# Optimization experiments

Measured on AMD Instinct MI355X. Metric: run time of the kernel, lower is better.

## Reference

```python
import jax, jax.numpy as jnp
import numpy as np

B, N, F_DIM, E, C = 8, 16384, 64, 262144, 10
BN_EPS = 1e-5


def setup_inputs() -> dict:
    key = jax.random.key(0)
    ks = jax.random.split(key, 10)
    s = 1.0 / np.sqrt(F_DIM)
    return {
        "x": jax.random.normal(ks[0], (B, N, F_DIM), jnp.float32),
        "edge_src": jax.random.randint(ks[1], (B, E), 0, N, jnp.int32),
        "edge_dst": jax.random.randint(ks[2], (B, E), 0, N, jnp.int32),
        "W1": jax.random.normal(ks[3], (F_DIM, F_DIM), jnp.float32) * s,
        "b1": jax.random.normal(ks[4], (F_DIM,), jnp.float32) * 0.01,
        "W2": jax.random.normal(ks[5], (F_DIM, F_DIM), jnp.float32) * s,
        "b2": jax.random.normal(ks[6], (F_DIM,), jnp.float32) * 0.01,
        "bn_gamma": jnp.ones((F_DIM,), jnp.float32),
        "bn_beta": jnp.zeros((F_DIM,), jnp.float32),
        "lin_W": jax.random.normal(ks[7], (C, N * F_DIM), jnp.float32) * (1.0 / np.sqrt(N * F_DIM)),
        "lin_b": jax.random.normal(ks[8], (C,), jnp.float32) * 0.01,
    }


def _graph_conv(x, src, dst, W, b):
    # DGL GraphConv, norm='both', in_feats == out_feats (aggregate-first path):
    # h = D_in^{-1/2} * A * (D_out^{-1/2} * x) @ W + b, degrees clamped to >= 1.
    ones = jnp.ones((src.shape[0],), x.dtype)
    deg_out = jnp.maximum(jax.ops.segment_sum(ones, src, num_segments=N), 1.0)
    deg_in = jnp.maximum(jax.ops.segment_sum(ones, dst, num_segments=N), 1.0)
    xs = x * jax.lax.rsqrt(deg_out)[:, None]          # [N, F]
    agg = jax.ops.segment_sum(xs[src], dst, num_segments=N)  # gather + scatter-add
    rst = agg * jax.lax.rsqrt(deg_in)[:, None]
    return rst @ W + b


def reference(x, edge_src, edge_dst, W1, b1, W2, b2, bn_gamma, bn_beta, lin_W, lin_b):
    conv = jax.vmap(_graph_conv, in_axes=(0, 0, 0, None, None))
    h = jax.nn.relu(conv(x, edge_src, edge_dst, W1, b1))  # conv1 + relu
    # dropout p=0.0 (eval): identity
    h = conv(h, edge_src, edge_dst, W2, b2)               # conv2 -> [B, N, F]
    # BatchNorm1d over channel F (torch normalizes over B and N in training mode)
    mean = jnp.mean(h, axis=(0, 1))
    var = jnp.var(h, axis=(0, 1))
    h = bn_gamma * (h - mean) * jax.lax.rsqrt(var + BN_EPS) + bn_beta
    flat = h.reshape(B, N * F_DIM)
    return flat @ lin_W.T + lin_b                         # [B, C]
```

## Files before the change

### kernel.cpp

```cpp
#include <hip/hip_runtime.h>

#define B_     8
#define N_     16384
#define F_     64
#define E_     262144
#define C_     10
#define NF_    (N_ * F_)
#define BN_    (B_ * N_)
#define BNF_   (B_ * N_ * F_)
#define BE_    (B_ * E_)
#define CAP_   48
#define CHUNK_ 4096
#define NCH_   (E_ / CHUNK_)
#define NW_    (N_ / 4)
#define NSB_   2048
#define NFB_   1024
#define EPS_   1e-5f

typedef _Float16 h8 __attribute__((ext_vector_type(8)));
typedef _Float16 h4 __attribute__((ext_vector_type(4)));

__global__ __launch_bounds__(256) void k_count(const int* __restrict__ src,
                                               const int* __restrict__ dst,
                                               unsigned int* __restrict__ partO,
                                               unsigned int* __restrict__ partI) {
    __shared__ unsigned int pO[NW_];
    __shared__ unsigned int pI[NW_];
    int t = threadIdx.x;
    int b = blockIdx.x & 7, c = blockIdx.x >> 3;
    for (int i = t; i < NW_; i += 256) { pO[i] = 0; pI[i] = 0; }
    __syncthreads();
    const int* sb = src + (size_t)b * E_ + (size_t)c * CHUNK_;
    const int* db = dst + (size_t)b * E_ + (size_t)c * CHUNK_;
    for (int i = t; i < CHUNK_; i += 256) {
        int s = sb[i], d = db[i];
        atomicAdd(&pO[s >> 2], 1u << ((s & 3) * 8));
        atomicAdd(&pI[d >> 2], 1u << ((d & 3) * 8));
    }
    __syncthreads();
    size_t base = (size_t)(b * NCH_ + c) * NW_;
    for (int i = t; i < NW_; i += 256) {
        partO[base + i] = pO[i];
        partI[base + i] = pI[i];
    }
}

__global__ __launch_bounds__(256) void k_offsets(const unsigned int* __restrict__ partO,
                                                 const unsigned int* __restrict__ partI,
                                                 unsigned int* __restrict__ baseArr,
                                                 float* __restrict__ degOr,
                                                 float* __restrict__ degIr,
                                                 int* __restrict__ cntI_g) {
    int gw = blockIdx.x * 256 + threadIdx.x;
    int b = gw >> 12;
    int rw = gw & 4095;
    unsigned int sumI = 0, sumO = 0;
    for (int c = 0; c < NCH_; ++c) {
        size_t idx = (size_t)(b * NCH_ + c) * NW_ + rw;
        unsigned int wI = partI[idx];
        baseArr[idx] = sumI;
        sumI += wI;
        sumO += partO[idx];
    }
    int row0 = gw * 4;
#pragma unroll
    for (int r = 0; r < 4; ++r) {
        unsigned int ci = (sumI >> (r * 8)) & 0xFFu;
        unsigned int co = (sumO >> (r * 8)) & 0xFFu;
        degIr[row0 + r] = rsqrtf(fmaxf((float)ci, 1.0f));
        degOr[row0 + r] = rsqrtf(fmaxf((float)co, 1.0f));
        cntI_g[row0 + r] = (int)ci;
    }
}

__global__ __launch_bounds__(256) void k_fill(const int* __restrict__ src,
                                              const int* __restrict__ dst,
                                              const unsigned int* __restrict__ baseArr,
                                              unsigned short* __restrict__ csr) {
    __shared__ unsigned int cur[NW_];
    __shared__ unsigned int bw[NW_];
    int t = threadIdx.x;
    int b = blockIdx.x & 7, c = blockIdx.x >> 3;
    size_t pbase = (size_t)(b * NCH_ + c) * NW_;
    for (int i = t; i < NW_; i += 256) { cur[i] = 0; bw[i] = baseArr[pbase + i]; }
    __syncthreads();
    const int* sb = src + (size_t)b * E_ + (size_t)c * CHUNK_;
    const int* db = dst + (size_t)b * E_ + (size_t)c * CHUNK_;
    unsigned short* cb = csr + (size_t)b * N_ * CAP_;
    for (int i = t; i < CHUNK_; i += 256) {
        int s = sb[i], d = db[i];
        unsigned int sh = (d & 3) * 8;
        unsigned int old = atomicAdd(&cur[d >> 2], 1u << sh);
        unsigned int pos = ((old >> sh) & 0xFFu) + ((bw[d >> 2] >> sh) & 0xFFu);
        if (pos < CAP_) cb[d * CAP_ + pos] = (unsigned short)s;
    }
}

template <bool SCALE, bool IN16, bool OUT16>
__global__ __launch_bounds__(256) void k_mmd(const float* __restrict__ in32,
                                             const _Float16* __restrict__ in16,
                                             const float* __restrict__ W,
                                             const float* __restrict__ rs,
                                             float* __restrict__ out32,
                                             _Float16* __restrict__ out16) {
    __shared__ float Wl[4096];
    __shared__ float4 rows[16][16];
    int t = threadIdx.x;
    int b = blockIdx.x & 7;
    int rowg = b * N_ + (blockIdx.x >> 3) * 16;
    for (int i = t; i < 1024; i += 256) ((float4*)Wl)[i] = ((const float4*)W)[i];
    {
        int rr = t >> 4, g = t & 15;
        if (IN16) {
            h4 hv = *(const h4*)(in16 + (size_t)(rowg + rr) * 64 + g * 4);
            rows[rr][g] = make_float4((float)hv[0], (float)hv[1], (float)hv[2], (float)hv[3]);
        } else {
            rows[rr][g] = ((const float4*)(in32 + (size_t)(rowg + rr) * 64))[g];
        }
    }
    __syncthreads();
    int f = t & 63;
    int wv = t >> 6;
    float a0 = 0.0f, a1 = 0.0f, a2 = 0.0f, a3 = 0.0f;
#pragma unroll
    for (int kg = 0; kg < 16; ++kg) {
        float4 r0 = rows[wv * 4 + 0][kg];
        float4 r1 = rows[wv * 4 + 1][kg];
        float4 r2 = rows[wv * 4 + 2][kg];
        float4 r3 = rows[wv * 4 + 3][kg];
        float w0 = Wl[(kg * 4 + 0) * 64 + f];
        float w1 = Wl[(kg * 4 + 1) * 64 + f];
        float w2 = Wl[(kg * 4 + 2) * 64 + f];
        float w3 = Wl[(kg * 4 + 3) * 64 + f];
        a0 = fmaf(r0.x, w0, a0); a0 = fmaf(r0.y, w1, a0); a0 = fmaf(r0.z, w2, a0); a0 = fmaf(r0.w, w3, a0);
        a1 = fmaf(r1.x, w0, a1); a1 = fmaf(r1.y, w1, a1); a1 = fmaf(r1.z, w2, a1); a1 = fmaf(r1.w, w3, a1);
        a2 = fmaf(r2.x, w0, a2); a2 = fmaf(r2.y, w1, a2); a2 = fmaf(r2.z, w2, a2); a2 = fmaf(r2.w, w3, a2);
        a3 = fmaf(r3.x, w0, a3); a3 = fmaf(r3.y, w1, a3); a3 = fmaf(r3.z, w2, a3); a3 = fmaf(r3.w, w3, a3);
    }
    int r0i = rowg + wv * 4;
    if (SCALE) {
        a0 *= rs[r0i]; a1 *= rs[r0i + 1]; a2 *= rs[r0i + 2]; a3 *= rs[r0i + 3];
    }
    if (OUT16) {
        out16[(size_t)(r0i + 0) * 64 + f] = (_Float16)a0;
        out16[(size_t)(r0i + 1) * 64 + f] = (_Float16)a1;
        out16[(size_t)(r0i + 2) * 64 + f] = (_Float16)a2;
        out16[(size_t)(r0i + 3) * 64 + f] = (_Float16)a3;
    } else {
        out32[(size_t)(r0i + 0) * 64 + f] = a0;
        out32[(size_t)(r0i + 1) * 64 + f] = a1;
        out32[(size_t)(r0i + 2) * 64 + f] = a2;
        out32[(size_t)(r0i + 3) * 64 + f] = a3;
    }
}

template <bool CONV1>
__global__ __launch_bounds__(256, 6) void k_gat(
        const int* __restrict__ cnt, const unsigned short* __restrict__ csr,
        const _Float16* __restrict__ z, const float* __restrict__ degIr,
        const float* __restrict__ degOr, const float* __restrict__ bias,
        _Float16* __restrict__ out16, float* __restrict__ out32) {
    int t = threadIdx.x;
    int lane = t & 63;
    int wave = t >> 6;
    int c8 = lane & 7;
    int b = blockIdx.x & 7;
    int row = (blockIdx.x >> 3) * 32 + wave * 8 + (lane >> 3);
    int wid = b * N_ + row;
    const _Float16* zb = z + (size_t)b * NF_;
    int lb = lane & 56;
    int ho = c8 * 8;

    int n = cnt[wid];
    if (n > CAP_) n = CAP_;
    size_t cb = (size_t)wid * CAP_;
    int e0 = csr[cb + c8] & 0x3FFF;
    int e1 = csr[cb + 8 + c8] & 0x3FFF;
    int e2 = csr[cb + 16 + c8] & 0x3FFF;
    int e3 = csr[cb + 24 + c8] & 0x3FFF;
    int e4 = csr[cb + 32 + c8] & 0x3FFF;
    int e5 = csr[cb + 40 + c8] & 0x3FFF;
    float dIr = degIr[wid];
    float4 bv0 = *(const float4*)(bias + ho);
    float4 bv1 = *(const float4*)(bias + ho + 4);
    int m = n;
    m = max(m, __shfl_xor(m, 8));
    m = max(m, __shfl_xor(m, 16));
    m = max(m, __shfl_xor(m, 32));

    float af[8];
#pragma unroll
    for (int i = 0; i < 8; ++i) af[i] = 0.0f;

#define SEG(EREG, KOFF)                                                        \
    {                                                                          \
        int rem = n - (KOFF);                                                  \
        h8 v[8];                                                               \
        _Pragma("unroll")                                                      \
        for (int jj = 0; jj < 8; ++jj) {                                       \
            int s = __shfl(EREG, lb + jj);                                     \
            h8 vv = {};                                                        \
            if (jj < rem) vv = *(const h8*)(zb + s * 64 + ho);                 \
            v[jj] = vv;                                                        \
        }                                                                      \
        h8 s0 = v[0] + v[1], s1 = v[2] + v[3];                                 \
        h8 s2 = v[4] + v[5], s3 = v[6] + v[7];                                 \
        h8 s4 = s0 + s1, s5 = s2 + s3;                                         \
        h8 s6 = s4 + s5;                                                       \
        _Pragma("unroll")                                                      \
        for (int i = 0; i < 8; ++i) af[i] += (float)s6[i];                     \
    }

    SEG(e0, 0)
    if (m > 8)  SEG(e1, 8)
    if (m > 16) SEG(e2, 16)
    if (m > 24) SEG(e3, 24)
    if (m > 32) SEG(e4, 32)
    if (m > 40) SEG(e5, 40)
#undef SEG

    float bb[8] = {bv0.x, bv0.y, bv0.z, bv0.w, bv1.x, bv1.y, bv1.z, bv1.w};
    if (CONV1) {
        float po = degOr[wid];
        h8 ov;
#pragma unroll
        for (int i = 0; i < 8; ++i) {
            ov[i] = (_Float16)(fmaxf(fmaf(af[i], dIr, bb[i]), 0.0f) * po);
        }
        *(h8*)(out16 + (size_t)wid * 64 + ho) = ov;
    } else {
        float4 o0, o1;
        o0.x = fmaf(af[0], dIr, bb[0]); o0.y = fmaf(af[1], dIr, bb[1]);
        o0.z = fmaf(af[2], dIr, bb[2]); o0.w = fmaf(af[3], dIr, bb[3]);
        o1.x = fmaf(af[4], dIr, bb[4]); o1.y = fmaf(af[5], dIr, bb[5]);
        o1.z = fmaf(af[6], dIr, bb[6]); o1.w = fmaf(af[7], dIr, bb[7]);
        float* op = out32 + (size_t)wid * 64 + ho;
        *(float4*)op = o0;
        *(float4*)(op + 4) = o1;
    }
}

__global__ __launch_bounds__(256) void k_stats2(const float* __restrict__ h,
                                                float* __restrict__ part) {
    int t = threadIdx.x;
    int base = blockIdx.x * (BNF_ / NSB_);
    float s = 0.0f, q = 0.0f;
#pragma unroll 4
    for (int k = 0; k < 16; ++k) {
        float v = h[(size_t)base + k * 256 + t];
        s += v;
        q += v * v;
    }
    __shared__ float ls[256], lq[256];
    ls[t] = s;
    lq[t] = q;
    __syncthreads();
    if (t < 64) {
        s = ls[t] + ls[t + 64] + ls[t + 128] + ls[t + 192];
        q = lq[t] + lq[t + 64] + lq[t + 128] + lq[t + 192];
        float* p = part + (size_t)blockIdx.x * 128;
        p[t] = s;
        p[64 + t] = q;
    }
}

__global__ __launch_bounds__(256) void k_red(const float* __restrict__ part,
                                             float* __restrict__ stats2) {
    __shared__ float sred[256];
    int t = threadIdx.x;
    int half = t >> 7;
    int s = t & 127;
    int r0 = blockIdx.x * (NSB_ / 32);
    float acc = 0.0f;
    for (int k = 0; k < NSB_ / 32 / 2; ++k) {
        acc += part[(size_t)(r0 + k * 2 + half) * 128 + s];
    }
    sred[t] = acc;
    __syncthreads();
    if (t < 128) stats2[blockIdx.x * 128 + t] = sred[t] + sred[t + 128];
}

__global__ void k_bnfin(const float* __restrict__ stats2, const float* __restrict__ gamma,
                        const float* __restrict__ beta, float* __restrict__ sc,
                        float* __restrict__ sh) {
    int f = threadIdx.x;
    if (f < 64) {
        float sum = 0.0f, sq = 0.0f;
        for (int j = 0; j < 32; ++j) {
            sum += stats2[j * 128 + f];
            sq  += stats2[j * 128 + 64 + f];
        }
        float inv = 1.0f / (float)BN_;
        float mean = sum * inv;
        float var  = sq * inv - mean * mean;
        float s = gamma[f] * rsqrtf(var + EPS_);
        sc[f] = s;
        sh[f] = beta[f] - mean * s;
    }
}

__global__ __launch_bounds__(256) void k_final(
        const float* __restrict__ h, const float* __restrict__ linW,
        const float* __restrict__ sc, const float* __restrict__ sh,
        float* __restrict__ pf) {
    int t = threadIdx.x;
    int lane = t & 63;
    int wv = t >> 6;
    int b0 = wv * 2, b1 = wv * 2 + 1;
    int base = blockIdx.x * (NF_ / NFB_);
    float s = sc[lane], shv = sh[lane];
    float acc[C_][2];
#pragma unroll
    for (int c = 0; c < C_; ++c) { acc[c][0] = 0.0f; acc[c][1] = 0.0f; }

#pragma unroll 4
    for (int k = 0; k < 16; ++k) {
        int i = base + k * 64 + lane;
        float h0 = fmaf(h[(size_t)b0 * NF_ + i], s, shv);
        float h1 = fmaf(h[(size_t)b1 * NF_ + i], s, shv);
#pragma unroll
        for (int c = 0; c < C_; ++c) {
            float w = linW[(size_t)c * NF_ + i];
            acc[c][0] = fmaf(h0, w, acc[c][0]);
            acc[c][1] = fmaf(h1, w, acc[c][1]);
        }
    }

#pragma unroll
    for (int c = 0; c < C_; ++c) {
#pragma unroll
        for (int j = 0; j < 2; ++j) {
            float v = acc[c][j];
            v += __shfl_down(v, 32);
            v += __shfl_down(v, 16);
            v += __shfl_down(v, 8);
            v += __shfl_down(v, 4);
            v += __shfl_down(v, 2);
            v += __shfl_down(v, 1);
            acc[c][j] = v;
        }
    }
    if (lane == 0) {
        float* p = pf + (size_t)blockIdx.x * 80;
#pragma unroll
        for (int c = 0; c < C_; ++c) {
            p[b0 * C_ + c] = acc[c][0];
            p[b1 * C_ + c] = acc[c][1];
        }
    }
}

__global__ __launch_bounds__(64) void k_fsum(const float* __restrict__ pf,
                                             const float* __restrict__ linb,
                                             float* __restrict__ out) {
    int o = blockIdx.x;
    int lane = threadIdx.x;
    float acc = 0.0f;
#pragma unroll
    for (int k = 0; k < 16; ++k) {
        acc += pf[(size_t)(k * 64 + lane) * 80 + o];
    }
    acc += __shfl_down(acc, 32);
    acc += __shfl_down(acc, 16);
    acc += __shfl_down(acc, 8);
    acc += __shfl_down(acc, 4);
    acc += __shfl_down(acc, 2);
    acc += __shfl_down(acc, 1);
    if (lane == 0) out[o] = acc + linb[o % C_];
}

extern "C" void kernel_launch(void* const* d_in, const int* in_sizes, int n_in,
                              void* d_out, int out_size, void* d_ws, size_t ws_size,
                              hipStream_t stream) {
    const float* x        = (const float*)d_in[0];
    const int*   edge_src = (const int*)d_in[1];
    const int*   edge_dst = (const int*)d_in[2];
    const float* W1       = (const float*)d_in[3];
    const float* b1       = (const float*)d_in[4];
    const float* W2       = (const float*)d_in[5];
    const float* b2       = (const float*)d_in[6];
    const float* gamma    = (const float*)d_in[7];
    const float* beta     = (const float*)d_in[8];
    const float* linW     = (const float*)d_in[9];
    const float* linb     = (const float*)d_in[10];
    float* out = (float*)d_out;

    char* w = (char*)d_ws;
    float* degOr = (float*)w;           w += BN_ * 4;
    float* degIr = (float*)w;           w += BN_ * 4;
    int*   cntI  = (int*)w;             w += BN_ * 4;
    unsigned short* csr = (unsigned short*)w; w += (size_t)BN_ * CAP_ * 2;
    _Float16* z    = (_Float16*)w;      w += (size_t)BNF_ * 2;
    _Float16* h1z  = (_Float16*)w;      w += (size_t)BNF_ * 2;
    float* h2    = (float*)w;           w += (size_t)BNF_ * 4;
    float* statPart = (float*)w;        w += (size_t)NSB_ * 128 * 4;
    float* stats2 = (float*)w;          w += 32 * 128 * 4;
    float* pf    = (float*)w;           w += (size_t)NFB_ * 80 * 4;
    float* sc    = (float*)w;           w += 64 * 4;
    float* sh    = (float*)w;           w += 64 * 4;

    unsigned int* partO   = (unsigned int*)h2;
    unsigned int* partI   = partO + (size_t)B_ * NCH_ * NW_;
    unsigned int* baseArr = (unsigned int*)z;

    k_count<<<B_ * NCH_, 256, 0, stream>>>(edge_src, edge_dst, partO, partI);
    k_offsets<<<BN_ / 4 / 256, 256, 0, stream>>>(partO, partI, baseArr, degOr, degIr, cntI);
    k_fill<<<B_ * NCH_, 256, 0, stream>>>(edge_src, edge_dst, baseArr, csr);

    k_mmd<true, false, true><<<BN_ / 16, 256, 0, stream>>>(x, nullptr, W1, degOr, nullptr, z);
    k_gat<true><<<BN_ / 32, 256, 0, stream>>>(cntI, csr, z, degIr, degOr, b1, h1z, nullptr);

    k_mmd<false, true, true><<<BN_ / 16, 256, 0, stream>>>(nullptr, h1z, W2, nullptr, nullptr, z);
    k_gat<false><<<BN_ / 32, 256, 0, stream>>>(cntI, csr, z, degIr, nullptr, b2, nullptr, h2);

    k_stats2<<<NSB_, 256, 0, stream>>>(h2, statPart);
    k_red<<<32, 256, 0, stream>>>(statPart, stats2);
    k_bnfin<<<1, 64, 0, stream>>>(stats2, gamma, beta, sc, sh);
    k_final<<<NFB_, 256, 0, stream>>>(h2, linW, sc, sh, pf);
    k_fsum<<<80, 64, 0, stream>>>(pf, linb, out);
}
```

Before: 280.8 us.

## Use MFMA f16 for feature transforms and fuse BN stats into conv2 gather

```diff
diff --git a/kernel.cpp b/kernel.cpp
--- a/kernel.cpp
+++ b/kernel.cpp
@@ -13,20 +13,38 @@
 #define CHUNK_ 4096
 #define NCH_   (E_ / CHUNK_)
 #define NW_    (N_ / 4)
-#define NSB_   2048
+#define NSB_   4096
 #define NFB_   1024
 #define EPS_   1e-5f
 
 typedef _Float16 h8 __attribute__((ext_vector_type(8)));
 typedef _Float16 h4 __attribute__((ext_vector_type(4)));
+typedef float f32x4 __attribute__((ext_vector_type(4)));
+
+#define SWZ(r, o) ((((r) * 64 + (o))) ^ (((r) & 7) << 3))
 
 __global__ __launch_bounds__(256) void k_count(const int* __restrict__ src,
                                                const int* __restrict__ dst,
                                                unsigned int* __restrict__ partO,
-                                               unsigned int* __restrict__ partI) {
+                                               unsigned int* __restrict__ partI,
+                                               const float* __restrict__ W1,
+                                               const float* __restrict__ W2,
+                                               _Float16* __restrict__ Wt1,
+                                               _Float16* __restrict__ Wt2) {
     __shared__ unsigned int pO[NW_];
     __shared__ unsigned int pI[NW_];
     int t = threadIdx.x;
+    if (blockIdx.x >= B_ * NCH_) {
+        int g = blockIdx.x - B_ * NCH_;
+        const float* Ws = (g & 8) ? W2 : W1;
+        _Float16* Wd = (g & 8) ? Wt2 : Wt1;
+        int c0 = (g & 7) * 512;
+        for (int j = t; j < 512; j += 256) {
+            int o = c0 + j;
+            Wd[o] = (_Float16)Ws[(o & 63) * 64 + (o >> 6)];
+        }
+        return;
+    }
     int b = blockIdx.x & 7, c = blockIdx.x >> 3;
     for (int i = t; i < NW_; i += 256) { pO[i] = 0; pI[i] = 0; }
     __syncthreads();
@@ -96,62 +114,76 @@
     }
 }
 
-template <bool SCALE, bool IN16, bool OUT16>
-__global__ __launch_bounds__(256) void k_mmd(const float* __restrict__ in32,
+template <bool IN16, bool SCALE>
+__global__ __launch_bounds__(256) void k_mmf(const float* __restrict__ in32,
                                              const _Float16* __restrict__ in16,
-                                             const float* __restrict__ W,
+                                             const _Float16* __restrict__ Wt,
                                              const float* __restrict__ rs,
-                                             float* __restrict__ out32,
-                                             _Float16* __restrict__ out16) {
-    __shared__ float Wl[4096];
-    __shared__ float4 rows[16][16];
-    int t = threadIdx.x;
-    int b = blockIdx.x & 7;
-    int rowg = b * N_ + (blockIdx.x >> 3) * 16;
-    for (int i = t; i < 1024; i += 256) ((float4*)Wl)[i] = ((const float4*)W)[i];
-    {
-        int rr = t >> 4, g = t & 15;
-        if (IN16) {
-            h4 hv = *(const h4*)(in16 + (size_t)(rowg + rr) * 64 + g * 4);
-            rows[rr][g] = make_float4((float)hv[0], (float)hv[1], (float)hv[2], (float)hv[3]);
+                                             _Float16* __restrict__ out) {
+    __shared__ _Float16 Al[4096];
+    __shared__ _Float16 Bl[4096];
+    int t = threadIdx.x;
+    int bat = blockIdx.x & 7;
+    int rowg = bat * N_ + (blockIdx.x >> 3) * 64;
+
+#pragma unroll
+    for (int j = 0; j < 2; ++j) {
+        int c = t + j * 256;
+        int r = c >> 3, o = (c & 7) * 8;
+        *(h8*)&Al[SWZ(r, o)] = *(const h8*)(Wt + c * 8);
+    }
+#pragma unroll
+    for (int j = 0; j < 2; ++j) {
+        int c = t + j * 256;
+        int r = c >> 3, o = (c & 7) * 8;
+        h8 v;
+        if constexpr (IN16) {
+            v = *(const h8*)(in16 + (size_t)(rowg + r) * 64 + o);
         } else {
-            rows[rr][g] = ((const float4*)(in32 + (size_t)(rowg + rr) * 64))[g];
-        }
+            const float4* p = (const float4*)(in32 + (size_t)(rowg + r) * 64 + o);
+            float4 x0 = p[0], x1 = p[1];
+            v[0] = (_Float16)x0.x; v[1] = (_Float16)x0.y;
+            v[2] = (_Float16)x0.z; v[3] = (_Float16)x0.w;
+            v[4] = (_Float16)x1.x; v[5] = (_Float16)x1.y;
+            v[6] = (_Float16)x1.z; v[7] = (_Float16)x1.w;
+        }
+        *(h8*)&Bl[SWZ(r, o)] = v;
     }
     __syncthreads();
-    int f = t & 63;
-    int wv = t >> 6;
-    float a0 = 0.0f, a1 = 0.0f, a2 = 0.0f, a3 = 0.0f;
-#pragma unroll
-    for (int kg = 0; kg < 16; ++kg) {
-        float4 r0 = rows[wv * 4 + 0][kg];
-        float4 r1 = rows[wv * 4 + 1][kg];
-        float4 r2 = rows[wv * 4 + 2][kg];
-        float4 r3 = rows[wv * 4 + 3][kg];
-        float w0 = Wl[(kg * 4 + 0) * 64 + f];
-        float w1 = Wl[(kg * 4 + 1) * 64 + f];
-        float w2 = Wl[(kg * 4 + 2) * 64 + f];
-        float w3 = Wl[(kg * 4 + 3) * 64 + f];
-        a0 = fmaf(r0.x, w0, a0); a0 = fmaf(r0.y, w1, a0); a0 = fmaf(r0.z, w2, a0); a0 = fmaf(r0.w, w3, a0);
-        a1 = fmaf(r1.x, w0, a1); a1 = fmaf(r1.y, w1, a1); a1 = fmaf(r1.z, w2, a1); a1 = fmaf(r1.w, w3, a1);
-        a2 = fmaf(r2.x, w0, a2); a2 = fmaf(r2.y, w1, a2); a2 = fmaf(r2.z, w2, a2); a2 = fmaf(r2.w, w3, a2);
-        a3 = fmaf(r3.x, w0, a3); a3 = fmaf(r3.y, w1, a3); a3 = fmaf(r3.z, w2, a3); a3 = fmaf(r3.w, w3, a3);
-    }
-    int r0i = rowg + wv * 4;
-    if (SCALE) {
-        a0 *= rs[r0i]; a1 *= rs[r0i + 1]; a2 *= rs[r0i + 2]; a3 *= rs[r0i + 3];
-    }
-    if (OUT16) {
-        out16[(size_t)(r0i + 0) * 64 + f] = (_Float16)a0;
-        out16[(size_t)(r0i + 1) * 64 + f] = (_Float16)a1;
-        out16[(size_t)(r0i + 2) * 64 + f] = (_Float16)a2;
-        out16[(size_t)(r0i + 3) * 64 + f] = (_Float16)a3;
-    } else {
-        out32[(size_t)(r0i + 0) * 64 + f] = a0;
-        out32[(size_t)(r0i + 1) * 64 + f] = a1;
-        out32[(size_t)(r0i + 2) * 64 + f] = a2;
-        out32[(size_t)(r0i + 3) * 64 + f] = a3;
-    }
+
+    int lane = t & 63;
+    int w = t >> 6;
+    int lm = lane & 15;
+    int lk = (lane >> 4) * 8;
+    f32x4 acc0 = {0.f, 0.f, 0.f, 0.f}, acc1 = {0.f, 0.f, 0.f, 0.f};
+    f32x4 acc2 = {0.f, 0.f, 0.f, 0.f}, acc3 = {0.f, 0.f, 0.f, 0.f};
+#pragma unroll
+    for (int ks = 0; ks < 2; ++ks) {
+        h8 a = *(const h8*)&Al[SWZ(w * 16 + lm, lk + ks * 32)];
+        h8 vb0 = *(const h8*)&Bl[SWZ(0 + lm, lk + ks * 32)];
+        h8 vb1 = *(const h8*)&Bl[SWZ(16 + lm, lk + ks * 32)];
+        h8 vb2 = *(const h8*)&Bl[SWZ(32 + lm, lk + ks * 32)];
+        h8 vb3 = *(const h8*)&Bl[SWZ(48 + lm, lk + ks * 32)];
+        acc0 = __builtin_amdgcn_mfma_f32_16x16x32_f16(a, vb0, acc0, 0, 0, 0);
+        acc1 = __builtin_amdgcn_mfma_f32_16x16x32_f16(a, vb1, acc1, 0, 0, 0);
+        acc2 = __builtin_amdgcn_mfma_f32_16x16x32_f16(a, vb2, acc2, 0, 0, 0);
+        acc3 = __builtin_amdgcn_mfma_f32_16x16x32_f16(a, vb3, acc3, 0, 0, 0);
+    }
+    int fo = w * 16 + (lane >> 4) * 4;
+#define STORE_TILE(ACC, RT)                                                    \
+    {                                                                          \
+        int row = rowg + (RT) * 16 + lm;                                       \
+        float scv = SCALE ? rs[row] : 1.0f;                                    \
+        h4 ov;                                                                 \
+        ov[0] = (_Float16)(ACC[0] * scv); ov[1] = (_Float16)(ACC[1] * scv);    \
+        ov[2] = (_Float16)(ACC[2] * scv); ov[3] = (_Float16)(ACC[3] * scv);    \
+        *(h4*)(out + (size_t)row * 64 + fo) = ov;                              \
+    }
+    STORE_TILE(acc0, 0)
+    STORE_TILE(acc1, 1)
+    STORE_TILE(acc2, 2)
+    STORE_TILE(acc3, 3)
+#undef STORE_TILE
 }
 
 template <bool CONV1>
@@ -159,7 +191,9 @@
         const int* __restrict__ cnt, const unsigned short* __restrict__ csr,
         const _Float16* __restrict__ z, const float* __restrict__ degIr,
         const float* __restrict__ degOr, const float* __restrict__ bias,
-        _Float16* __restrict__ out16, float* __restrict__ out32) {
+        _Float16* __restrict__ out16, float* __restrict__ pstat) {
+    __shared__ float sS[4][64];
+    __shared__ float sQ[4][64];
     int t = threadIdx.x;
     int lane = t & 63;
     int wave = t >> 6;
@@ -220,7 +254,7 @@
 #undef SEG
 
     float bb[8] = {bv0.x, bv0.y, bv0.z, bv0.w, bv1.x, bv1.y, bv1.z, bv1.w};
-    if (CONV1) {
+    if constexpr (CONV1) {
         float po = degOr[wid];
         h8 ov;
 #pragma unroll
@@ -229,38 +263,37 @@
         }
         *(h8*)(out16 + (size_t)wid * 64 + ho) = ov;
     } else {
-        float4 o0, o1;
-        o0.x = fmaf(af[0], dIr, bb[0]); o0.y = fmaf(af[1], dIr, bb[1]);
-        o0.z = fmaf(af[2], dIr, bb[2]); o0.w = fmaf(af[3], dIr, bb[3]);
-        o1.x = fmaf(af[4], dIr, bb[4]); o1.y = fmaf(af[5], dIr, bb[5]);
-        o1.z = fmaf(af[6], dIr, bb[6]); o1.w = fmaf(af[7], dIr, bb[7]);
-        float* op = out32 + (size_t)wid * 64 + ho;
-        *(float4*)op = o0;
-        *(float4*)(op + 4) = o1;
-    }
-}
-
-__global__ __launch_bounds__(256) void k_stats2(const float* __restrict__ h,
-                                                float* __restrict__ part) {
-    int t = threadIdx.x;
-    int base = blockIdx.x * (BNF_ / NSB_);
-    float s = 0.0f, q = 0.0f;
-#pragma unroll 4
-    for (int k = 0; k < 16; ++k) {
-        float v = h[(size_t)base + k * 256 + t];
-        s += v;
-        q += v * v;
-    }
-    __shared__ float ls[256], lq[256];
-    ls[t] = s;
-    lq[t] = q;
-    __syncthreads();
-    if (t < 64) {
-        s = ls[t] + ls[t + 64] + ls[t + 128] + ls[t + 192];
-        q = lq[t] + lq[t + 64] + lq[t + 128] + lq[t + 192];
-        float* p = part + (size_t)blockIdx.x * 128;
-        p[t] = s;
-        p[64 + t] = q;
+        float vv[8];
+        h8 ov;
+#pragma unroll
+        for (int i = 0; i < 8; ++i) {
+            vv[i] = fmaf(af[i], dIr, bb[i]);
+            ov[i] = (_Float16)vv[i];
+        }
+        *(h8*)(out16 + (size_t)wid * 64 + ho) = ov;
+        float ssv[8], qqv[8];
+#pragma unroll
+        for (int i = 0; i < 8; ++i) { ssv[i] = vv[i]; qqv[i] = vv[i] * vv[i]; }
+#pragma unroll
+        for (int i = 0; i < 8; ++i) {
+            ssv[i] += __shfl_xor(ssv[i], 8);  qqv[i] += __shfl_xor(qqv[i], 8);
+            ssv[i] += __shfl_xor(ssv[i], 16); qqv[i] += __shfl_xor(qqv[i], 16);
+            ssv[i] += __shfl_xor(ssv[i], 32); qqv[i] += __shfl_xor(qqv[i], 32);
+        }
+        if (lane < 8) {
+#pragma unroll
+            for (int i = 0; i < 8; ++i) {
+                sS[wave][lane * 8 + i] = ssv[i];
+                sQ[wave][lane * 8 + i] = qqv[i];
+            }
+        }
+        __syncthreads();
+        if (t < 64) {
+            float s_ = sS[0][t] + sS[1][t] + sS[2][t] + sS[3][t];
+            float q_ = sQ[0][t] + sQ[1][t] + sQ[2][t] + sQ[3][t];
+            pstat[(size_t)blockIdx.x * 128 + t] = s_;
+            pstat[(size_t)blockIdx.x * 128 + 64 + t] = q_;
+        }
     }
 }
 
@@ -300,7 +333,7 @@
 }
 
 __global__ __launch_bounds__(256) void k_final(
-        const float* __restrict__ h, const float* __restrict__ linW,
+        const _Float16* __restrict__ h, const float* __restrict__ linW,
         const float* __restrict__ sc, const float* __restrict__ sh,
         float* __restrict__ pf) {
     int t = threadIdx.x;
@@ -316,8 +349,8 @@
 #pragma unroll 4
     for (int k = 0; k < 16; ++k) {
         int i = base + k * 64 + lane;
-        float h0 = fmaf(h[(size_t)b0 * NF_ + i], s, shv);
-        float h1 = fmaf(h[(size_t)b1 * NF_ + i], s, shv);
+        float h0 = fmaf((float)h[(size_t)b0 * NF_ + i], s, shv);
+        float h1 = fmaf((float)h[(size_t)b1 * NF_ + i], s, shv);
 #pragma unroll
         for (int c = 0; c < C_; ++c) {
             float w = linW[(size_t)c * NF_ + i];
@@ -392,30 +425,31 @@
     unsigned short* csr = (unsigned short*)w; w += (size_t)BN_ * CAP_ * 2;
     _Float16* z    = (_Float16*)w;      w += (size_t)BNF_ * 2;
     _Float16* h1z  = (_Float16*)w;      w += (size_t)BNF_ * 2;
-    float* h2    = (float*)w;           w += (size_t)BNF_ * 4;
-    float* statPart = (float*)w;        w += (size_t)NSB_ * 128 * 4;
+    _Float16* h2h  = (_Float16*)w;      w += (size_t)BNF_ * 2;
+    unsigned int* partO   = (unsigned int*)w;  w += (size_t)B_ * NCH_ * NW_ * 4;
+    unsigned int* partI   = (unsigned int*)w;  w += (size_t)B_ * NCH_ * NW_ * 4;
+    unsigned int* baseArr = (unsigned int*)w;  w += (size_t)B_ * NCH_ * NW_ * 4;
+    float* partStats = (float*)w;       w += (size_t)NSB_ * 128 * 4;
     float* stats2 = (float*)w;          w += 32 * 128 * 4;
     float* pf    = (float*)w;           w += (size_t)NFB_ * 80 * 4;
     float* sc    = (float*)w;           w += 64 * 4;
     float* sh    = (float*)w;           w += 64 * 4;
-
-    unsigned int* partO   = (unsigned int*)h2;
-    unsigned int* partI   = partO + (size_t)B_ * NCH_ * NW_;
-    unsigned int* baseArr = (unsigned int*)z;
-
-    k_count<<<B_ * NCH_, 256, 0, stream>>>(edge_src, edge_dst, partO, partI);
+    _Float16* Wt1 = (_Float16*)w;       w += 4096 * 2;
+    _Float16* Wt2 = (_Float16*)w;       w += 4096 * 2;
+
+    k_count<<<B_ * NCH_ + 16, 256, 0, stream>>>(edge_src, edge_dst, partO, partI,
+                                                W1, W2, Wt1, Wt2);
     k_offsets<<<BN_ / 4 / 256, 256, 0, stream>>>(partO, partI, baseArr, degOr, degIr, cntI);
     k_fill<<<B_ * NCH_, 256, 0, stream>>>(edge_src, edge_dst, baseArr, csr);
 
-    k_mmd<true, false, true><<<BN_ / 16, 256, 0, stream>>>(x, nullptr, W1, degOr, nullptr, z);
+    k_mmf<false, true><<<BN_ / 64, 256, 0, stream>>>(x, nullptr, Wt1, degOr, z);
     k_gat<true><<<BN_ / 32, 256, 0, stream>>>(cntI, csr, z, degIr, degOr, b1, h1z, nullptr);
 
-    k_mmd<false, true, true><<<BN_ / 16, 256, 0, stream>>>(nullptr, h1z, W2, nullptr, nullptr, z);
-    k_gat<false><<<BN_ / 32, 256, 0, stream>>>(cntI, csr, z, degIr, nullptr, b2, nullptr, h2);
-
-    k_stats2<<<NSB_, 256, 0, stream>>>(h2, statPart);
-    k_red<<<32, 256, 0, stream>>>(statPart, stats2);
+    k_mmf<true, false><<<BN_ / 64, 256, 0, stream>>>(nullptr, h1z, Wt2, nullptr, z);
+    k_gat<false><<<BN_ / 32, 256, 0, stream>>>(cntI, csr, z, degIr, nullptr, b2, h2h, partStats);
+
+    k_red<<<32, 256, 0, stream>>>(partStats, stats2);
     k_bnfin<<<1, 64, 0, stream>>>(stats2, gamma, beta, sc, sh);
-    k_final<<<NFB_, 256, 0, stream>>>(h2, linW, sc, sh, pf);
+    k_final<<<NFB_, 256, 0, stream>>>(h2h, linW, sc, sh, pf);
     k_fsum<<<80, 64, 0, stream>>>(pf, linb, out);
 }
```

Measured after the change: 239.2 us. 1.17x faster.
